# Kernel optimization log

Measured on AMD Instinct MI355X. Metric: run time of the kernel, lower is better.

## Reference

```python
import jax, jax.numpy as jnp
import numpy as np

NUM_CLASSES = 91
FEAT_DIM = 256
N = 131072
MOMENTUM = 0.999
WARMUP_STEPS = 200
BASE_MOM = 0.99


def setup_inputs() -> dict:
    key = jax.random.key(0)
    ks = jax.random.split(key, 8)
    return {
        "features": jax.random.normal(ks[0], (N, FEAT_DIM), dtype=jnp.float32),
        "labels": jax.random.randint(ks[1], (N,), 0, NUM_CLASSES, dtype=jnp.int32),
        "prototypes": jax.random.normal(ks[2], (NUM_CLASSES, FEAT_DIM), dtype=jnp.float32),
        "proto_initialized": jax.random.randint(ks[3], (NUM_CLASSES,), 0, 2).astype(bool),
        "proto_variance": jax.random.uniform(ks[4], (NUM_CLASSES,), dtype=jnp.float32),
        "shadow_prototypes": jax.random.normal(ks[5], (NUM_CLASSES, FEAT_DIM), dtype=jnp.float32),
        "shadow_initialized": jax.random.randint(ks[6], (NUM_CLASSES,), 0, 2).astype(bool),
        "proto_update_count": jax.random.randint(ks[7], (NUM_CLASSES,), 0, 1000, dtype=jnp.int64) if jax.config.jax_enable_x64 else jax.random.randint(ks[7], (NUM_CLASSES,), 0, 1000, dtype=jnp.int32),
        "step": 500,
    }


def reference(features, labels, prototypes, proto_initialized, proto_variance,
              shadow_prototypes, shadow_initialized, proto_update_count, step):
    C, D = prototypes.shape
    # L2-normalize features (F.normalize, eps=1e-12)
    f = features / jnp.clip(jnp.linalg.norm(features, axis=-1, keepdims=True), 1e-12)
    # per-class segment mean (the gather-reduce the torch loop does per unique label)
    sums = jax.ops.segment_sum(f, labels, num_segments=C)            # [C, D]
    counts = jax.ops.segment_sum(jnp.ones(labels.shape, f.dtype), labels, num_segments=C)  # [C]
    present = counts > 0                                              # classes in this batch
    cls_feat = sums / jnp.maximum(counts, 1.0)[:, None]               # [C, D]

    # adaptive per-class momentum (_get_momentum, vectorized)
    progress = min(1.0, float(step) / max(1, WARMUP_STEPS * 10))
    mom = jnp.where(proto_initialized,
                    BASE_MOM + (MOMENTUM - BASE_MOM) * jnp.exp(-proto_variance) * progress,
                    BASE_MOM)                                         # [C]

    old = prototypes
    ema = mom[:, None] * old + (1.0 - mom[:, None]) * cls_feat
    new_proto = jnp.where(present[:, None],
                          jnp.where(proto_initialized[:, None], ema, cls_feat),
                          old)

    # variance EMA on update magnitude (only for already-initialized present classes)
    diff = cls_feat - old
    upd_mag = jnp.sqrt(jnp.sum(diff * diff, axis=-1) + 1e-24)         # [C]
    new_var = jnp.where(present & proto_initialized,
                        0.99 * proto_variance + 0.01 * upd_mag,
                        proto_variance)

    # shadow (dual) prototype EMA — uses the UPDATED prototype, as in the torch loop
    shadow_m = min(MOMENTUM + 0.0009, 0.9999)
    shadow_ema = shadow_m * shadow_prototypes + (1.0 - shadow_m) * new_proto
    new_shadow = jnp.where(present[:, None],
                           jnp.where(shadow_initialized[:, None], shadow_ema, new_proto),
                           shadow_prototypes)

    new_initialized = proto_initialized | present
    new_shadow_init = shadow_initialized | present
    new_count = proto_update_count + present.astype(proto_update_count.dtype)
    return (new_proto, new_var, new_shadow, new_initialized, new_shadow_init, new_count)
```

## Files before the change

kernel.cpp:

```cpp
#include <hip/hip_runtime.h>
#include <math.h>

#define NCLS 91
#define FDIM 256
#define NB   256
#define BINSZ  (NCLS * FDIM)
#define BINSZP (92 * FDIM)
#define NRED 8

typedef float f32x4 __attribute__((ext_vector_type(4)));
typedef short short8 __attribute__((ext_vector_type(8)));

__device__ __forceinline__ float wave_sum64(float ss) {
    #pragma unroll
    for (int m = 1; m < 64; m <<= 1) ss += __shfl_xor(ss, m, 64);
    return ss;
}
__device__ __forceinline__ int wave_sum64_i(int v) {
    #pragma unroll
    for (int m = 1; m < 64; m <<= 1) v += __shfl_xor(v, m, 64);
    return v;
}

template <int CTRL>
__device__ __forceinline__ float dpp_addstep(float v) {
    return v + __int_as_float(__builtin_amdgcn_mov_dpp(
        __float_as_int(v), CTRL, 0xf, 0xf, true));
}
__device__ __forceinline__ float group16_sum(float v) {
    v = dpp_addstep<0xB1>(v);
    v = dpp_addstep<0x1B>(v);
    v = dpp_addstep<0x141>(v);
    v = dpp_addstep<0x140>(v);
    return v;
}

__device__ __forceinline__ unsigned short f2bf(float x) {
    unsigned u = __float_as_uint(x);
    return (unsigned short)((u + 0x7FFFu + ((u >> 16) & 1u)) >> 16);
}
__device__ __forceinline__ float bf2f(unsigned short h) {
    return __uint_as_float((unsigned)h << 16);
}

#define MPT 1024
#define CHUNK 64
#define ROWSTRIDE 260

extern "C" __global__ void __launch_bounds__(MPT)
mfma_main(const float* __restrict__ feats, const int* __restrict__ labels,
          unsigned short* __restrict__ slices, unsigned int* __restrict__ cnts_ws,
          int nrows, int rpb)
{
    __shared__ __align__(16) unsigned short sdat[2][CHUNK * ROWSTRIDE];
    __shared__ __align__(8)  unsigned char  slbl[2][CHUNK];
    __shared__ unsigned int scnt[96];

    const int tid  = threadIdx.x;
    const int lane = tid & 63;
    const int w    = tid >> 6;
    const int l16  = lane & 15;
    const int g    = lane >> 4;
    const int d0   = w * 16;
    const int r_loc = w * 4 + g;

    if (tid < 96) scnt[tid] = 0u;

    const int row0 = blockIdx.x * rpb;
    const int nch  = rpb / CHUNK;

    f32x4 acc[6];
    #pragma unroll
    for (int ct = 0; ct < 6; ++ct) acc[ct] = (f32x4){0.f, 0.f, 0.f, 0.f};

    float4 A0, A1, A2, A3; int labA;
    float4 B0, B1, B2, B3; int labB;

    auto loadA = [&](int ch) {
        const int r = row0 + ch * CHUNK + r_loc;
        if (r < nrows) {
            const float4* bp = (const float4*)(feats + (size_t)r * FDIM + l16 * 16);
            A0 = bp[0]; A1 = bp[1]; A2 = bp[2]; A3 = bp[3];
            labA = labels[r];
        } else {
            A0 = A1 = A2 = A3 = make_float4(0.f, 0.f, 0.f, 0.f);
            labA = 255;
        }
    };
    auto loadB = [&](int ch) {
        const int r = row0 + ch * CHUNK + r_loc;
        if (r < nrows) {
            const float4* bp = (const float4*)(feats + (size_t)r * FDIM + l16 * 16);
            B0 = bp[0]; B1 = bp[1]; B2 = bp[2]; B3 = bp[3];
            labB = labels[r];
        } else {
            B0 = B1 = B2 = B3 = make_float4(0.f, 0.f, 0.f, 0.f);
            labB = 255;
        }
    };

    auto stage = [&](int buf, const float4& p0, const float4& p1,
                     const float4& p2, const float4& p3, int plab) {
        float ss = 0.f;
        ss = fmaf(p0.x, p0.x, ss); ss = fmaf(p0.y, p0.y, ss);
        ss = fmaf(p0.z, p0.z, ss); ss = fmaf(p0.w, p0.w, ss);
        ss = fmaf(p1.x, p1.x, ss); ss = fmaf(p1.y, p1.y, ss);
        ss = fmaf(p1.z, p1.z, ss); ss = fmaf(p1.w, p1.w, ss);
        ss = fmaf(p2.x, p2.x, ss); ss = fmaf(p2.y, p2.y, ss);
        ss = fmaf(p2.z, p2.z, ss); ss = fmaf(p2.w, p2.w, ss);
        ss = fmaf(p3.x, p3.x, ss); ss = fmaf(p3.y, p3.y, ss);
        ss = fmaf(p3.z, p3.z, ss); ss = fmaf(p3.w, p3.w, ss);
        ss = group16_sum(ss);
        const float inv = 1.0f / fmaxf(sqrtf(ss), 1e-12f);
        unsigned long long* q =
            (unsigned long long*)&sdat[buf][0] + (size_t)r_loc * 65 + l16 * 4;
        const float e[16] = {p0.x, p0.y, p0.z, p0.w, p1.x, p1.y, p1.z, p1.w,
                             p2.x, p2.y, p2.z, p2.w, p3.x, p3.y, p3.z, p3.w};
        #pragma unroll
        for (int t = 0; t < 4; ++t) {
            unsigned long long v =
                (unsigned long long)f2bf(e[4 * t + 0] * inv)
              | ((unsigned long long)f2bf(e[4 * t + 1] * inv) << 16)
              | ((unsigned long long)f2bf(e[4 * t + 2] * inv) << 32)
              | ((unsigned long long)f2bf(e[4 * t + 3] * inv) << 48);
            q[t] = v;
        }
        if (l16 == 0) {
            slbl[buf][r_loc] = (unsigned char)plab;
            if (plab < 96) atomicAdd(&scnt[plab], 1u);
        }
    };

    auto mfma_phase = [&](int buf) {
        #pragma unroll
        for (int s = 0; s < 2; ++s) {
            const int kbase = s * 32 + g * 8;
            const unsigned long long lb =
                *(const unsigned long long*)&slbl[buf][kbase];
            int la[8];
            #pragma unroll
            for (int j = 0; j < 8; ++j) la[j] = (int)((lb >> (8 * j)) & 0xFFu);

            short8 b;
            #pragma unroll
            for (int j = 0; j < 8; ++j)
                b[j] = (short)sdat[buf][(size_t)(kbase + j) * ROWSTRIDE + d0 + l16];

            #pragma unroll
            for (int ct = 0; ct < 6; ++ct) {
                const int c = ct * 16 + l16;
                short8 a;
                #pragma unroll
                for (int j = 0; j < 8; ++j)
                    a[j] = (la[j] == c) ? (short)0x3F80 : (short)0;
                acc[ct] = __builtin_amdgcn_mfma_f32_16x16x32_bf16(a, b, acc[ct], 0, 0, 0);
            }
        }
    };

    loadA(0);
    __syncthreads();
    stage(0, A0, A1, A2, A3, labA);
    loadA(1);
    __syncthreads();

    for (int p = 0; p < nch; p += 2) {
        if (p + 2 < nch) loadB(p + 2);
        mfma_phase(0);
        stage(1, A0, A1, A2, A3, labA);
        __syncthreads();

        if (p + 3 < nch) loadA(p + 3);
        mfma_phase(1);
        if (p + 2 < nch) stage(0, B0, B1, B2, B3, labB);
        __syncthreads();
    }

    unsigned short* es = &sdat[0][0];
    #pragma unroll
    for (int ct = 0; ct < 6; ++ct) {
        #pragma unroll
        for (int reg = 0; reg < 4; ++reg) {
            const int c = ct * 16 + g * 4 + reg;
            if (c < NCLS)
                es[c * FDIM + d0 + l16] = f2bf(acc[ct][reg]);
        }
    }
    __syncthreads();
    {
        const unsigned long long* src = (const unsigned long long*)es;
        unsigned long long* dst =
            (unsigned long long*)(slices + (size_t)blockIdx.x * BINSZP);
        for (int i = tid; i < BINSZ / 4; i += MPT) dst[i] = src[i];
    }
    if (tid < 96) cnts_ws[(size_t)blockIdx.x * 96 + tid] = scnt[tid];
}

extern "C" __global__ void __launch_bounds__(FDIM)
reduce_k(const unsigned short* __restrict__ slices, float* __restrict__ part2)
{
    const int t4 = blockIdx.x;
    const int h  = blockIdx.y;
    const int t  = threadIdx.x;
    const int off = t4 * 1024 + t * 4;
    const int p0 = h * (NB / NRED);

    float s0 = 0.f, s1 = 0.f, s2 = 0.f, s3 = 0.f;
    #pragma unroll 1
    for (int p = 0; p < NB / NRED; p += 4) {
        #pragma unroll
        for (int u = 0; u < 4; ++u) {
            const unsigned long long v = *(const unsigned long long*)
                (slices + (size_t)(p0 + p + u) * BINSZP + off);
            s0 += bf2f((unsigned short)(v));
            s1 += bf2f((unsigned short)(v >> 16));
            s2 += bf2f((unsigned short)(v >> 32));
            s3 += bf2f((unsigned short)(v >> 48));
        }
    }
    float4* dst = (float4*)(part2 + (size_t)h * BINSZP + off);
    *dst = make_float4(s0, s1, s2, s3);
}

__device__ int detect_bool_enc(const void* p) {
    const unsigned int* u = (const unsigned int*)p;
    bool i32ok = true, f32ok = true;
    for (int i = 0; i < 22; ++i) {
        unsigned int w = u[i];
        if (w > 1u) i32ok = false;
        if (w != 0u && w != 0x3F800000u) f32ok = false;
    }
    return i32ok ? 1 : (f32ok ? 2 : 0);
}
__device__ bool read_bool(const void* p, int enc, int i) {
    if (enc == 1) return ((const unsigned int*)p)[i] != 0u;
    if (enc == 2) return ((const float*)p)[i] != 0.0f;
    return ((const unsigned char*)p)[i] != 0;
}
__device__ int read_step(const void* p) {
    unsigned int w = ((const unsigned int*)p)[0];
    int iv = (int)w;
    if (iv >= 0 && iv < 16777216) return iv;
    return (int)__uint_as_float(w);
}

extern "C" __global__ void __launch_bounds__(FDIM)
final_k(const float* __restrict__ part2, const unsigned int* __restrict__ cnts_ws,
        const float* __restrict__ protos, const void* __restrict__ p_init,
        const float* __restrict__ p_var, const float* __restrict__ shadow,
        const void* __restrict__ s_init, const int* __restrict__ p_count,
        const void* __restrict__ p_step, float* __restrict__ out)
{
    const int c = blockIdx.x;
    const int d = threadIdx.x;

    __shared__ int enc_pi, enc_si;
    __shared__ float red[FDIM / 64];
    __shared__ int credi[FDIM / 64];
    __shared__ float s_upd;
    __shared__ unsigned int s_cnt;
    if (d == 0) { enc_pi = detect_bool_enc(p_init); enc_si = detect_bool_enc(s_init); }

    int cpart = 0;
    for (int p = d; p < NB; p += FDIM)
        cpart += (int)cnts_ws[(size_t)p * 96 + c];
    int cw = wave_sum64_i(cpart);
    if ((d & 63) == 0) credi[d >> 6] = cw;
    __syncthreads();
    if (d == 0) s_cnt = (unsigned int)(credi[0] + credi[1] + credi[2] + credi[3]);

    const int slot = c * FDIM + d;
    float sum = 0.f;
    #pragma unroll
    for (int h = 0; h < NRED; ++h) sum += part2[(size_t)h * BINSZP + slot];
    __syncthreads();

    const unsigned int cnt = s_cnt;
    const bool present = cnt > 0u;
    const float cls = sum / fmaxf((float)cnt, 1.0f);
    const float oldp = protos[c * FDIM + d];

    const float diff = cls - oldp;
    float ds = wave_sum64(diff * diff);
    if ((d & 63) == 0) red[d >> 6] = ds;
    __syncthreads();
    if (d == 0) s_upd = sqrtf(red[0] + red[1] + red[2] + red[3] + 1e-24f);
    __syncthreads();
    const float upd_mag = s_upd;

    const bool  init  = read_bool(p_init, enc_pi, c);
    const bool  sinit = read_bool(s_init, enc_si, c);
    const float var   = p_var[c];
    const int   step  = read_step(p_step);

    const float progress = fminf(1.0f, (float)step * (1.0f / 2000.0f));
    const float mom = init ? (0.99f + 0.009f * expf(-var) * progress) : 0.99f;

    const float ema   = mom * oldp + (1.0f - mom) * cls;
    const float newp  = present ? (init ? ema : cls) : oldp;

    const float sh     = shadow[c * FDIM + d];
    const float sh_ema = 0.9999f * sh + 0.0001f * newp;
    const float newsh  = present ? (sinit ? sh_ema : newp) : sh;

    const int O1 = NCLS * FDIM;
    const int O2 = O1 + NCLS;
    const int O3 = O2 + NCLS * FDIM;
    const int O4 = O3 + NCLS;
    const int O5 = O4 + NCLS;

    out[c * FDIM + d]       = newp;
    out[O2 + c * FDIM + d]  = newsh;
    if (d == 0) {
        const float newvar = (present && init) ? (0.99f * var + 0.01f * upd_mag) : var;
        out[O1 + c] = newvar;
        out[O3 + c] = (init || present)  ? 1.0f : 0.0f;
        out[O4 + c] = (sinit || present) ? 1.0f : 0.0f;
        out[O5 + c] = (float)(p_count[c] + (present ? 1 : 0));
    }
}

extern "C" void kernel_launch(void* const* d_in, const int* in_sizes, int n_in,
                              void* d_out, int out_size, void* d_ws, size_t ws_size,
                              hipStream_t stream) {
    const float* feats  = (const float*)d_in[0];
    const int*   labels = (const int*)d_in[1];
    const float* protos = (const float*)d_in[2];
    const void*  p_init = d_in[3];
    const float* p_var  = (const float*)d_in[4];
    const float* shadow = (const float*)d_in[5];
    const void*  s_init = d_in[6];
    const int*   p_cnt  = (const int*)d_in[7];
    const void*  p_step = d_in[8];
    const int nrows = in_sizes[1];

    int rpb = (nrows + NB - 1) / NB;
    rpb = ((rpb + 2 * CHUNK - 1) / (2 * CHUNK)) * (2 * CHUNK);

    unsigned short* slices  = (unsigned short*)d_ws;
    unsigned int*   cnts_ws = (unsigned int*)((char*)d_ws + (size_t)BINSZP * NB * 2);
    float*          part2   = (float*)((char*)d_ws + (size_t)BINSZP * NB * 2
                                       + (size_t)NB * 96 * 4);

    mfma_main<<<NB, MPT, 0, stream>>>(feats, labels, slices, cnts_ws, nrows, rpb);
    reduce_k<<<dim3(23, NRED), FDIM, 0, stream>>>(slices, part2);
    final_k<<<NCLS, FDIM, 0, stream>>>(part2, cnts_ws, protos, p_init, p_var,
                                       shadow, s_init, p_cnt, p_step, (float*)d_out);
}
```

Measured before the change: 49.68 us.

## Use 512 smaller blocks with two MFMA accumulators per wave and nontemporal loads

Doubles the block count to 512 and halves threads per block to 512, with 32-row chunks. Each wave now covers 32 feature columns using two accumulator sets, so every one-hot A fragment feeds two MFMAs. The pipeline becomes a single prefetch register set with a one-chunk lookahead, and feature loads are marked nontemporal. The aim is better occupancy and latency hiding in the main kernel, but the number of per-block bf16 partial slices doubles, which adds workspace traffic and work for the reduction kernel.

```diff
diff --git a/kernel.cpp b/kernel.cpp
--- a/kernel.cpp
+++ b/kernel.cpp
@@ -3,7 +3,7 @@
 
 #define NCLS 91
 #define FDIM 256
-#define NB   256
+#define NB   512
 #define BINSZ  (NCLS * FDIM)
 #define BINSZP (92 * FDIM)
 #define NRED 8
@@ -43,8 +43,8 @@
     return __uint_as_float((unsigned)h << 16);
 }
 
-#define MPT 1024
-#define CHUNK 64
+#define MPT 512
+#define CHUNK 32
 #define ROWSTRIDE 260
 
 extern "C" __global__ void __launch_bounds__(MPT)
@@ -61,70 +61,69 @@
     const int w    = tid >> 6;
     const int l16  = lane & 15;
     const int g    = lane >> 4;
-    const int d0   = w * 16;
-    const int r_loc = w * 4 + g;
+    const int d0   = w * 32;
+    const int r_loc = tid >> 4;
 
     if (tid < 96) scnt[tid] = 0u;
 
     const int row0 = blockIdx.x * rpb;
     const int nch  = rpb / CHUNK;
 
-    f32x4 acc[6];
-    #pragma unroll
-    for (int ct = 0; ct < 6; ++ct) acc[ct] = (f32x4){0.f, 0.f, 0.f, 0.f};
-
-    float4 A0, A1, A2, A3; int labA;
-    float4 B0, B1, B2, B3; int labB;
-
-    auto loadA = [&](int ch) {
+    f32x4 accA[6], accB[6];
+    #pragma unroll
+    for (int ct = 0; ct < 6; ++ct) {
+        accA[ct] = (f32x4){0.f, 0.f, 0.f, 0.f};
+        accB[ct] = (f32x4){0.f, 0.f, 0.f, 0.f};
+    }
+
+    f32x4 pf0, pf1, pf2, pf3;
+    int plab;
+
+    auto prefetch = [&](int ch) {
         const int r = row0 + ch * CHUNK + r_loc;
         if (r < nrows) {
-            const float4* bp = (const float4*)(feats + (size_t)r * FDIM + l16 * 16);
-            A0 = bp[0]; A1 = bp[1]; A2 = bp[2]; A3 = bp[3];
-            labA = labels[r];
+            const f32x4* bp = (const f32x4*)(feats + (size_t)r * FDIM + l16 * 16);
+            pf0 = __builtin_nontemporal_load(bp);
+            pf1 = __builtin_nontemporal_load(bp + 1);
+            pf2 = __builtin_nontemporal_load(bp + 2);
+            pf3 = __builtin_nontemporal_load(bp + 3);
+            plab = labels[r];
         } else {
-            A0 = A1 = A2 = A3 = make_float4(0.f, 0.f, 0.f, 0.f);
-            labA = 255;
+            pf0 = pf1 = pf2 = pf3 = (f32x4){0.f, 0.f, 0.f, 0.f};
+            plab = 255;
         }
     };
-    auto loadB = [&](int ch) {
-        const int r = row0 + ch * CHUNK + r_loc;
-        if (r < nrows) {
-            const float4* bp = (const float4*)(feats + (size_t)r * FDIM + l16 * 16);
-            B0 = bp[0]; B1 = bp[1]; B2 = bp[2]; B3 = bp[3];
-            labB = labels[r];
-        } else {
-            B0 = B1 = B2 = B3 = make_float4(0.f, 0.f, 0.f, 0.f);
-            labB = 255;
-        }
-    };
-
-    auto stage = [&](int buf, const float4& p0, const float4& p1,
-                     const float4& p2, const float4& p3, int plab) {
+
+    auto stage = [&](int buf) {
         float ss = 0.f;
-        ss = fmaf(p0.x, p0.x, ss); ss = fmaf(p0.y, p0.y, ss);
-        ss = fmaf(p0.z, p0.z, ss); ss = fmaf(p0.w, p0.w, ss);
-        ss = fmaf(p1.x, p1.x, ss); ss = fmaf(p1.y, p1.y, ss);
-        ss = fmaf(p1.z, p1.z, ss); ss = fmaf(p1.w, p1.w, ss);
-        ss = fmaf(p2.x, p2.x, ss); ss = fmaf(p2.y, p2.y, ss);
-        ss = fmaf(p2.z, p2.z, ss); ss = fmaf(p2.w, p2.w, ss);
-        ss = fmaf(p3.x, p3.x, ss); ss = fmaf(p3.y, p3.y, ss);
-        ss = fmaf(p3.z, p3.z, ss); ss = fmaf(p3.w, p3.w, ss);
+        #pragma unroll
+        for (int k = 0; k < 4; ++k) ss = fmaf(pf0[k], pf0[k], ss);
+        #pragma unroll
+        for (int k = 0; k < 4; ++k) ss = fmaf(pf1[k], pf1[k], ss);
+        #pragma unroll
+        for (int k = 0; k < 4; ++k) ss = fmaf(pf2[k], pf2[k], ss);
+        #pragma unroll
+        for (int k = 0; k < 4; ++k) ss = fmaf(pf3[k], pf3[k], ss);
         ss = group16_sum(ss);
         const float inv = 1.0f / fmaxf(sqrtf(ss), 1e-12f);
         unsigned long long* q =
             (unsigned long long*)&sdat[buf][0] + (size_t)r_loc * 65 + l16 * 4;
-        const float e[16] = {p0.x, p0.y, p0.z, p0.w, p1.x, p1.y, p1.z, p1.w,
-                             p2.x, p2.y, p2.z, p2.w, p3.x, p3.y, p3.z, p3.w};
-        #pragma unroll
-        for (int t = 0; t < 4; ++t) {
-            unsigned long long v =
-                (unsigned long long)f2bf(e[4 * t + 0] * inv)
-              | ((unsigned long long)f2bf(e[4 * t + 1] * inv) << 16)
-              | ((unsigned long long)f2bf(e[4 * t + 2] * inv) << 32)
-              | ((unsigned long long)f2bf(e[4 * t + 3] * inv) << 48);
-            q[t] = v;
-        }
+        q[0] = (unsigned long long)f2bf(pf0[0] * inv)
+             | ((unsigned long long)f2bf(pf0[1] * inv) << 16)
+             | ((unsigned long long)f2bf(pf0[2] * inv) << 32)
+             | ((unsigned long long)f2bf(pf0[3] * inv) << 48);
+        q[1] = (unsigned long long)f2bf(pf1[0] * inv)
+             | ((unsigned long long)f2bf(pf1[1] * inv) << 16)
+             | ((unsigned long long)f2bf(pf1[2] * inv) << 32)
+             | ((unsigned long long)f2bf(pf1[3] * inv) << 48);
+        q[2] = (unsigned long long)f2bf(pf2[0] * inv)
+             | ((unsigned long long)f2bf(pf2[1] * inv) << 16)
+             | ((unsigned long long)f2bf(pf2[2] * inv) << 32)
+             | ((unsigned long long)f2bf(pf2[3] * inv) << 48);
+        q[3] = (unsigned long long)f2bf(pf3[0] * inv)
+             | ((unsigned long long)f2bf(pf3[1] * inv) << 16)
+             | ((unsigned long long)f2bf(pf3[2] * inv) << 32)
+             | ((unsigned long long)f2bf(pf3[3] * inv) << 48);
         if (l16 == 0) {
             slbl[buf][r_loc] = (unsigned char)plab;
             if (plab < 96) atomicAdd(&scnt[plab], 1u);
@@ -132,47 +131,46 @@
     };
 
     auto mfma_phase = [&](int buf) {
-        #pragma unroll
-        for (int s = 0; s < 2; ++s) {
-            const int kbase = s * 32 + g * 8;
-            const unsigned long long lb =
-                *(const unsigned long long*)&slbl[buf][kbase];
-            int la[8];
-            #pragma unroll
-            for (int j = 0; j < 8; ++j) la[j] = (int)((lb >> (8 * j)) & 0xFFu);
-
-            short8 b;
+        const int kbase = g * 8;
+        const unsigned long long lb =
+            *(const unsigned long long*)&slbl[buf][kbase];
+        int la[8];
+        #pragma unroll
+        for (int j = 0; j < 8; ++j) la[j] = (int)((lb >> (8 * j)) & 0xFFu);
+
+        short8 b0, b1;
+        #pragma unroll
+        for (int j = 0; j < 8; ++j) {
+            const unsigned short* rp = &sdat[buf][(size_t)(kbase + j) * ROWSTRIDE];
+            b0[j] = (short)rp[d0 + l16];
+            b1[j] = (short)rp[d0 + 16 + l16];
+        }
+
+        #pragma unroll
+        for (int ct = 0; ct < 6; ++ct) {
+            const int c = ct * 16 + l16;
+            short8 a;
             #pragma unroll
             for (int j = 0; j < 8; ++j)
-                b[j] = (short)sdat[buf][(size_t)(kbase + j) * ROWSTRIDE + d0 + l16];
-
-            #pragma unroll
-            for (int ct = 0; ct < 6; ++ct) {
-                const int c = ct * 16 + l16;
-                short8 a;
-                #pragma unroll
-                for (int j = 0; j < 8; ++j)
-                    a[j] = (la[j] == c) ? (short)0x3F80 : (short)0;
-                acc[ct] = __builtin_amdgcn_mfma_f32_16x16x32_bf16(a, b, acc[ct], 0, 0, 0);
-            }
+                a[j] = (la[j] == c) ? (short)0x3F80 : (short)0;
+            accA[ct] = __builtin_amdgcn_mfma_f32_16x16x32_bf16(a, b0, accA[ct], 0, 0, 0);
+            accB[ct] = __builtin_amdgcn_mfma_f32_16x16x32_bf16(a, b1, accB[ct], 0, 0, 0);
         }
     };
 
-    loadA(0);
-    __syncthreads();
-    stage(0, A0, A1, A2, A3, labA);
-    loadA(1);
-    __syncthreads();
-
-    for (int p = 0; p < nch; p += 2) {
-        if (p + 2 < nch) loadB(p + 2);
-        mfma_phase(0);
-        stage(1, A0, A1, A2, A3, labA);
-        __syncthreads();
-
-        if (p + 3 < nch) loadA(p + 3);
-        mfma_phase(1);
-        if (p + 2 < nch) stage(0, B0, B1, B2, B3, labB);
+    prefetch(0);
+    __syncthreads();
+    stage(0);
+    if (nch > 1) prefetch(1);
+    __syncthreads();
+
+    for (int ch = 0; ch < nch; ++ch) {
+        const int cur = ch & 1;
+        mfma_phase(cur);
+        if (ch + 1 < nch) {
+            stage(cur ^ 1);
+            if (ch + 2 < nch) prefetch(ch + 2);
+        }
         __syncthreads();
     }
 
@@ -182,8 +180,10 @@
         #pragma unroll
         for (int reg = 0; reg < 4; ++reg) {
             const int c = ct * 16 + g * 4 + reg;
-            if (c < NCLS)
-                es[c * FDIM + d0 + l16] = f2bf(acc[ct][reg]);
+            if (c < NCLS) {
+                es[c * FDIM + d0 + l16]      = f2bf(accA[ct][reg]);
+                es[c * FDIM + d0 + 16 + l16] = f2bf(accB[ct][reg]);
+            }
         }
     }
     __syncthreads();
@@ -335,7 +335,7 @@
     const int nrows = in_sizes[1];
 
     int rpb = (nrows + NB - 1) / NB;
-    rpb = ((rpb + 2 * CHUNK - 1) / (2 * CHUNK)) * (2 * CHUNK);
+    rpb = ((rpb + CHUNK - 1) / CHUNK) * CHUNK;
 
     unsigned short* slices  = (unsigned short*)d_ws;
     unsigned int*   cnts_ws = (unsigned int*)((char*)d_ws + (size_t)BINSZP * NB * 2);
```

Measured after the change: 63.84 us. 28.5% more time.
